# Kernel optimization log

Hardware: AMD Instinct MI355X
Metric: run time of the kernel (lower is better)

## Reference

```python
import jax, jax.numpy as jnp
import numpy as np
from jax import lax

# quantization bit widths (config)
IB, WB, RB, AB = 8, 4, 4, 8


def quantize(x, bw):
    """Signed fixed-point quantization to bw bits in [-1, 1) with STE."""
    scale = 2.0 ** (bw - 1)
    q = jnp.clip(jnp.round(x * scale), -scale, scale - 1) / scale
    return x + lax.stop_gradient(q - x)


def setup_inputs() -> dict:
    key = jax.random.key(0)
    k1, k2, k3, k4, k5 = jax.random.split(key, 5)
    B, T, I, H, O = 256, 1024, 64, 256, 16
    inputs = jax.random.normal(k1, (B, T, I), dtype=jnp.float32)
    # input kernel init: uniform(-1, 1)
    Wi = jax.random.uniform(k2, (H, I), dtype=jnp.float32, minval=-1.0, maxval=1.0)
    # recurrent kernel: orthogonal (geotorch parametrization); materialize via QR
    A = jax.random.normal(k3, (H, H), dtype=jnp.float32)
    Wr, _ = jnp.linalg.qr(A)
    Wr = Wr.astype(jnp.float32)
    Wo = jax.random.normal(k4, (O, H), dtype=jnp.float32) * 0.1
    b = jax.random.normal(k5, (H,), dtype=jnp.float32) * 0.01
    return {"inputs": inputs, "Wi": Wi, "Wr": Wr, "Wo": Wo, "b": b}


def reference(inputs, Wi, Wr, Wo, b):
    # quantize inputs (ib bits)
    x = quantize(inputs, IB)
    # quantized input projection, precomputed for all timesteps: [B,T,H]
    u = jnp.einsum("bti,hi->bth", x, quantize(Wi, WB))
    Wrq = quantize(Wr, RB)  # quantized orthogonal recurrent weight [H,H]
    B = inputs.shape[0]
    H = Wr.shape[0]
    h0 = jnp.zeros((B, H), dtype=inputs.dtype)

    def step(h, u_t):
        z = u_t + h @ Wrq.T                      # [B,H]
        m = jax.nn.relu(jnp.abs(z) + b)          # modrelu magnitude
        h_new = quantize(jnp.sign(z) * m, AB)    # quantized activation
        return h_new, None

    u_t = jnp.swapaxes(u, 0, 1)  # [T,B,H]
    h_last, _ = lax.scan(step, h0, u_t)
    # output head on last hidden state
    out = h_last @ quantize(Wo, WB).T  # [B,O]
    return out
```

## Files before the change

### kernel.cpp

```cpp
#include <hip/hip_runtime.h>


#define TSEQ 1024
#define IDIM 64
#define HDIM 256
#define ODIM 16

__device__ __forceinline__ int sdot4i8(int a, int b, int c) {
#if __has_builtin(__builtin_amdgcn_sdot4)
    return __builtin_amdgcn_sdot4(a, b, c, false);
#else
    int r = c;
    r += ((a << 24) >> 24) * ((b << 24) >> 24);
    r += ((a << 16) >> 24) * ((b << 16) >> 24);
    r += ((a << 8)  >> 24) * ((b << 8)  >> 24);
    r += (a >> 24) * (b >> 24);
    return r;
#endif
}

__device__ __forceinline__ int qpack4(float4 f, float s, float lo, float hi) {
    int a = (int)fminf(fmaxf(rintf(f.x * s), lo), hi);
    int b = (int)fminf(fmaxf(rintf(f.y * s), lo), hi);
    int c = (int)fminf(fmaxf(rintf(f.z * s), lo), hi);
    int d = (int)fminf(fmaxf(rintf(f.w * s), lo), hi);
    return (a & 255) | ((b & 255) << 8) | ((c & 255) << 16) | ((d & 255) << 24);
}

__device__ __forceinline__ int qsum(int v) {
    v += __builtin_amdgcn_update_dpp(0, v, 0xB1, 0xF, 0xF, true);
    v += __builtin_amdgcn_update_dpp(0, v, 0x4E, 0xF, 0xF, true);
    return v;
}

__global__ __launch_bounds__(256, 1)
void qornn_kernel(const float* __restrict__ x, const float* __restrict__ Wi,
                  const float* __restrict__ Wr, const float* __restrict__ Wo,
                  const float* __restrict__ bias, float* __restrict__ out) {
    __shared__ alignas(16) int xlds[TSEQ * 16 + 16];
    __shared__ alignas(16) int wstage[8192];
    __shared__ alignas(16) int hbuf[2][64];

    const int tid = threadIdx.x;
    const int brow = blockIdx.x;
    const int w    = tid >> 6;
    const int l    = tid & 63;
    const int q    = l & 3;
    const int m16  = l >> 2;
    const int obase = w * 64 + m16 * 4;

    {
        const float4* wi4 = (const float4*)Wi;
        #pragma unroll
        for (int it = 0; it < 16; ++it) {
            int flat = it * 256 + tid;
            wstage[flat] = qpack4(wi4[flat], 8.0f, -8.0f, 7.0f);
        }
    }
    __syncthreads();
    int4 wiq[4];
    {
        const int4* p = (const int4*)wstage;
        #pragma unroll
        for (int i = 0; i < 4; ++i) wiq[i] = p[(obase + i) * 4 + q];
    }
    __syncthreads();

    int4 wr[16];
    {
        const float4* wr4 = (const float4*)Wr;
        #pragma unroll
        for (int it = 0; it < 32; ++it) {
            int flat = it * 256 + tid;
            wstage[flat] = qpack4(wr4[flat], 8.0f, -8.0f, 7.0f);
        }
        __syncthreads();
        if (obase < 128) {
            const int4* p = (const int4*)wstage;
            #pragma unroll
            for (int i = 0; i < 4; ++i)
                #pragma unroll
                for (int r = 0; r < 4; ++r)
                    wr[i * 4 + r] = p[(obase + i) * 16 + q * 4 + r];
        }
        __syncthreads();
        #pragma unroll
        for (int it = 0; it < 32; ++it) {
            int flat = it * 256 + tid;
            wstage[flat] = qpack4(wr4[8192 + flat], 8.0f, -8.0f, 7.0f);
        }
        __syncthreads();
        if (obase >= 128) {
            const int4* p = (const int4*)wstage;
            #pragma unroll
            for (int i = 0; i < 4; ++i)
                #pragma unroll
                for (int r = 0; r < 4; ++r)
                    wr[i * 4 + r] = p[(obase - 128 + i) * 16 + q * 4 + r];
        }
        __syncthreads();
    }

    {
        const float4* wo4 = (const float4*)Wo;
        #pragma unroll
        for (int it = 0; it < 4; ++it) {
            int flat = it * 256 + tid;
            wstage[flat] = qpack4(wo4[flat], 8.0f, -8.0f, 7.0f);
        }
    }

    {
        const float4* rowf4 = (const float4*)(x + (size_t)brow * (TSEQ * IDIM));
        #pragma unroll 8
        for (int it = 0; it < 64; ++it) {
            int flat = it * 256 + tid;
            xlds[flat] = qpack4(rowf4[flat], 128.0f, -128.0f, 127.0f);
        }
    }
    if (tid < 64) hbuf[0][tid] = 0;
    __syncthreads();

    const float bv = bias[tid];
    const bool qb0 = (q & 1) != 0;
    const bool qb1 = (q & 2) != 0;

    int u[4];
    {
        const int4 xx = ((const int4*)xlds)[q];
        #pragma unroll
        for (int i = 0; i < 4; ++i) {
            int s = sdot4i8(xx.x, wiq[i].x, 0);
            s = sdot4i8(xx.y, wiq[i].y, s);
            s = sdot4i8(xx.z, wiq[i].z, s);
            u[i] = sdot4i8(xx.w, wiq[i].w, s);
        }
    }

    #pragma unroll 2
    for (int t = 0; t < TSEQ; ++t) {
        int4 hh[4];
        {
            const int4* hP = (const int4*)hbuf[t & 1];
            #pragma unroll
            for (int r = 0; r < 4; ++r) hh[r] = hP[q * 4 + r];
        }
        const int4 xn = ((const int4*)xlds)[(t + 1) * 4 + q];

        int za[4], zb[4];
        #pragma unroll
        for (int i = 0; i < 4; ++i) {
            int s0 = u[i];
            s0 = sdot4i8(hh[0].x, wr[i * 4 + 0].x, s0);
            s0 = sdot4i8(hh[0].y, wr[i * 4 + 0].y, s0);
            s0 = sdot4i8(hh[0].z, wr[i * 4 + 0].z, s0);
            s0 = sdot4i8(hh[0].w, wr[i * 4 + 0].w, s0);
            s0 = sdot4i8(hh[1].x, wr[i * 4 + 1].x, s0);
            s0 = sdot4i8(hh[1].y, wr[i * 4 + 1].y, s0);
            s0 = sdot4i8(hh[1].z, wr[i * 4 + 1].z, s0);
            s0 = sdot4i8(hh[1].w, wr[i * 4 + 1].w, s0);
            int s1 = 0;
            s1 = sdot4i8(hh[2].x, wr[i * 4 + 2].x, s1);
            s1 = sdot4i8(hh[2].y, wr[i * 4 + 2].y, s1);
            s1 = sdot4i8(hh[2].z, wr[i * 4 + 2].z, s1);
            s1 = sdot4i8(hh[2].w, wr[i * 4 + 2].w, s1);
            s1 = sdot4i8(hh[3].x, wr[i * 4 + 3].x, s1);
            s1 = sdot4i8(hh[3].y, wr[i * 4 + 3].y, s1);
            s1 = sdot4i8(hh[3].z, wr[i * 4 + 3].z, s1);
            s1 = sdot4i8(hh[3].w, wr[i * 4 + 3].w, s1);
            za[i] = s0; zb[i] = s1;
        }
        int un[4];
        #pragma unroll
        for (int i = 0; i < 4; ++i) {
            int s = sdot4i8(xn.x, wiq[i].x, 0);
            s = sdot4i8(xn.y, wiq[i].y, s);
            s = sdot4i8(xn.z, wiq[i].z, s);
            un[i] = sdot4i8(xn.w, wiq[i].w, s);
        }

        const int z0 = qsum(za[0] + zb[0]);
        const int z1 = qsum(za[1] + zb[1]);
        const int z2 = qsum(za[2] + zb[2]);
        const int z3 = qsum(za[3] + zb[3]);
        const int zlo = qb0 ? z1 : z0;
        const int zhi = qb0 ? z3 : z2;
        const int z   = qb1 ? zhi : zlo;

        const float zf = (float)z;
        const float t1 = fmaf(fabsf(zf), 0.0009765625f, bv);
        const float t2 = fmaxf(t1, 0.0f);
        const float r  = rintf(t2 * 128.0f);
        const int vpos = (int)fminf(r, 127.0f);
        const int vneg = -(int)fminf(r, 128.0f);
        int hv = (z < 0) ? vneg : vpos;
        hv = (z == 0) ? 0 : hv;

        ((signed char*)hbuf[(t + 1) & 1])[tid] = (signed char)hv;

        #pragma unroll
        for (int i = 0; i < 4; ++i) u[i] = un[i];
        __syncthreads();
    }

    if (tid < ODIM) {
        const int4* wo = (const int4*)wstage;
        const int4* hl = (const int4*)hbuf[0];
        int a0 = 0, a1 = 0, a2 = 0, a3 = 0;
        #pragma unroll
        for (int i = 0; i < 16; ++i) {
            int4 w4 = wo[tid * 16 + i];
            int4 h4 = hl[i];
            a0 = sdot4i8(h4.x, w4.x, a0);
            a1 = sdot4i8(h4.y, w4.y, a1);
            a2 = sdot4i8(h4.z, w4.z, a2);
            a3 = sdot4i8(h4.w, w4.w, a3);
        }
        out[brow * ODIM + tid] = (float)((a0 + a1) + (a2 + a3)) * 0.0009765625f;
    }
}

extern "C" void kernel_launch(void* const* d_in, const int* in_sizes, int n_in,
                              void* d_out, int out_size, void* d_ws, size_t ws_size,
                              hipStream_t stream) {
    const float* x  = (const float*)d_in[0];
    const float* Wi = (const float*)d_in[1];
    const float* Wr = (const float*)d_in[2];
    const float* Wo = (const float*)d_in[3];
    const float* b  = (const float*)d_in[4];
    float* out = (float*)d_out;

    const int B = in_sizes[0] / (TSEQ * IDIM);
    qornn_kernel<<<B, HDIM, 0, stream>>>(x, Wi, Wr, Wo, b, out);
}
```

Measured before the change: 423.1 us.

## Pack four batch rows per block and stream input chunks double-buffered

```diff
diff --git a/kernel.cpp b/kernel.cpp
--- a/kernel.cpp
+++ b/kernel.cpp
@@ -5,6 +5,9 @@
 #define IDIM 64
 #define HDIM 256
 #define ODIM 16
+#define RPW 4
+#define CHUNK 64
+#define NCHUNK (TSEQ / CHUNK)
 
 __device__ __forceinline__ int sdot4i8(int a, int b, int c) {
 #if __has_builtin(__builtin_amdgcn_sdot4)
@@ -33,27 +36,26 @@
     return v;
 }
 
-__global__ __launch_bounds__(256, 1)
+__global__ __launch_bounds__(1024, 1)
 void qornn_kernel(const float* __restrict__ x, const float* __restrict__ Wi,
                   const float* __restrict__ Wr, const float* __restrict__ Wo,
                   const float* __restrict__ bias, float* __restrict__ out) {
-    __shared__ alignas(16) int xlds[TSEQ * 16 + 16];
     __shared__ alignas(16) int wstage[8192];
-    __shared__ alignas(16) int hbuf[2][64];
-
-    const int tid = threadIdx.x;
-    const int brow = blockIdx.x;
-    const int w    = tid >> 6;
-    const int l    = tid & 63;
+    __shared__ alignas(16) int wo_lds[1024];
+    __shared__ alignas(16) int hbuf[RPW][2][64];
+
+    const int tid  = threadIdx.x;
+    const int g    = tid >> 8;
+    const int t256 = tid & 255;
+    const int l    = t256 & 63;
     const int q    = l & 3;
-    const int m16  = l >> 2;
-    const int obase = w * 64 + m16 * 4;
+    const int obase = (t256 >> 6) * 64 + (l >> 2) * 4;
 
     {
         const float4* wi4 = (const float4*)Wi;
         #pragma unroll
-        for (int it = 0; it < 16; ++it) {
-            int flat = it * 256 + tid;
+        for (int it = 0; it < 4; ++it) {
+            int flat = it * 1024 + tid;
             wstage[flat] = qpack4(wi4[flat], 8.0f, -8.0f, 7.0f);
         }
     }
@@ -70,64 +72,50 @@
     {
         const float4* wr4 = (const float4*)Wr;
         #pragma unroll
-        for (int it = 0; it < 32; ++it) {
-            int flat = it * 256 + tid;
-            wstage[flat] = qpack4(wr4[flat], 8.0f, -8.0f, 7.0f);
-        }
-        __syncthreads();
-        if (obase < 128) {
-            const int4* p = (const int4*)wstage;
+        for (int half = 0; half < 2; ++half) {
             #pragma unroll
-            for (int i = 0; i < 4; ++i)
+            for (int it = 0; it < 8; ++it) {
+                int flat = it * 1024 + tid;
+                wstage[flat] = qpack4(wr4[half * 8192 + flat], 8.0f, -8.0f, 7.0f);
+            }
+            __syncthreads();
+            if ((obase >> 7) == half) {
+                const int4* p = (const int4*)wstage;
+                const int ob = obase & 127;
                 #pragma unroll
-                for (int r = 0; r < 4; ++r)
-                    wr[i * 4 + r] = p[(obase + i) * 16 + q * 4 + r];
-        }
-        __syncthreads();
-        #pragma unroll
-        for (int it = 0; it < 32; ++it) {
-            int flat = it * 256 + tid;
-            wstage[flat] = qpack4(wr4[8192 + flat], 8.0f, -8.0f, 7.0f);
-        }
-        __syncthreads();
-        if (obase >= 128) {
-            const int4* p = (const int4*)wstage;
-            #pragma unroll
-            for (int i = 0; i < 4; ++i)
-                #pragma unroll
-                for (int r = 0; r < 4; ++r)
-                    wr[i * 4 + r] = p[(obase - 128 + i) * 16 + q * 4 + r];
-        }
-        __syncthreads();
+                for (int i = 0; i < 4; ++i)
+                    #pragma unroll
+                    for (int r = 0; r < 4; ++r)
+                        wr[i * 4 + r] = p[(ob + i) * 16 + q * 4 + r];
+            }
+            __syncthreads();
+        }
     }
 
     {
         const float4* wo4 = (const float4*)Wo;
+        wo_lds[tid] = qpack4(wo4[tid], 8.0f, -8.0f, 7.0f);
+    }
+
+    const int row = blockIdx.x * RPW + g;
+    const float4* rowf4 = (const float4*)(x + (size_t)row * (TSEQ * IDIM));
+    int* xg = wstage + g * 2048;
+    {
         #pragma unroll
         for (int it = 0; it < 4; ++it) {
-            int flat = it * 256 + tid;
-            wstage[flat] = qpack4(wo4[flat], 8.0f, -8.0f, 7.0f);
-        }
-    }
-
-    {
-        const float4* rowf4 = (const float4*)(x + (size_t)brow * (TSEQ * IDIM));
-        #pragma unroll 8
-        for (int it = 0; it < 64; ++it) {
-            int flat = it * 256 + tid;
-            xlds[flat] = qpack4(rowf4[flat], 128.0f, -128.0f, 127.0f);
-        }
-    }
-    if (tid < 64) hbuf[0][tid] = 0;
-    __syncthreads();
-
-    const float bv = bias[tid];
+            int idx = it * 256 + t256;
+            xg[idx] = qpack4(rowf4[idx], 128.0f, -128.0f, 127.0f);
+        }
+    }
+    if (t256 < 64) hbuf[g][0][t256] = 0;
+    const float bv = bias[t256];
     const bool qb0 = (q & 1) != 0;
     const bool qb1 = (q & 2) != 0;
+    __syncthreads();
 
     int u[4];
     {
-        const int4 xx = ((const int4*)xlds)[q];
+        const int4 xx = *(const int4*)(xg + q * 4);
         #pragma unroll
         for (int i = 0; i < 4; ++i) {
             int s = sdot4i8(xx.x, wiq[i].x, 0);
@@ -137,15 +125,25 @@
         }
     }
 
-    #pragma unroll 2
     for (int t = 0; t < TSEQ; ++t) {
+        if ((t & (CHUNK - 1)) == (g << 3) && t < TSEQ - CHUNK) {
+            const int nc = (t >> 6) + 1;
+            int* dst = xg + (nc & 1) * 1024;
+            #pragma unroll
+            for (int it = 0; it < 4; ++it) {
+                int idx = it * 256 + t256;
+                dst[idx] = qpack4(rowf4[nc * 1024 + idx], 128.0f, -128.0f, 127.0f);
+            }
+        }
+
         int4 hh[4];
         {
-            const int4* hP = (const int4*)hbuf[t & 1];
+            const int4* hP = (const int4*)hbuf[g][t & 1];
             #pragma unroll
             for (int r = 0; r < 4; ++r) hh[r] = hP[q * 4 + r];
         }
-        const int4 xn = ((const int4*)xlds)[(t + 1) * 4 + q];
+        const int tt = (t + 1) & (TSEQ - 1);
+        const int4 xn = *(const int4*)(xg + ((tt >> 6) & 1) * 1024 + (tt & 63) * 16 + q * 4);
 
         int za[4], zb[4];
         #pragma unroll
@@ -196,27 +194,27 @@
         int hv = (z < 0) ? vneg : vpos;
         hv = (z == 0) ? 0 : hv;
 
-        ((signed char*)hbuf[(t + 1) & 1])[tid] = (signed char)hv;
+        ((signed char*)hbuf[g][(t + 1) & 1])[t256] = (signed char)hv;
 
         #pragma unroll
         for (int i = 0; i < 4; ++i) u[i] = un[i];
         __syncthreads();
     }
 
-    if (tid < ODIM) {
-        const int4* wo = (const int4*)wstage;
-        const int4* hl = (const int4*)hbuf[0];
+    if (t256 < ODIM) {
+        const int4* wo = (const int4*)wo_lds;
+        const int4* hl = (const int4*)hbuf[g][0];
         int a0 = 0, a1 = 0, a2 = 0, a3 = 0;
         #pragma unroll
         for (int i = 0; i < 16; ++i) {
-            int4 w4 = wo[tid * 16 + i];
+            int4 w4 = wo[t256 * 16 + i];
             int4 h4 = hl[i];
             a0 = sdot4i8(h4.x, w4.x, a0);
             a1 = sdot4i8(h4.y, w4.y, a1);
             a2 = sdot4i8(h4.z, w4.z, a2);
             a3 = sdot4i8(h4.w, w4.w, a3);
         }
-        out[brow * ODIM + tid] = (float)((a0 + a1) + (a2 + a3)) * 0.0009765625f;
+        out[row * ODIM + t256] = (float)((a0 + a1) + (a2 + a3)) * 0.0009765625f;
     }
 }
 
@@ -231,5 +229,5 @@
     float* out = (float*)d_out;
 
     const int B = in_sizes[0] / (TSEQ * IDIM);
-    qornn_kernel<<<B, HDIM, 0, stream>>>(x, Wi, Wr, Wo, b, out);
-}
+    qornn_kernel<<<B / RPW, RPW * 256, 0, stream>>>(x, Wi, Wr, Wo, b, out);
+}
```

Result: slower. 1.091 ms (+158.0%).

## Double threads per block, halving output rows per quad in recurrence

Applied to the files above, without the earlier changes.

```diff
diff --git a/kernel.cpp b/kernel.cpp
--- a/kernel.cpp
+++ b/kernel.cpp
@@ -33,103 +33,88 @@
     return v;
 }
 
-__global__ __launch_bounds__(256, 1)
+__global__ __launch_bounds__(512, 2)
 void qornn_kernel(const float* __restrict__ x, const float* __restrict__ Wi,
                   const float* __restrict__ Wr, const float* __restrict__ Wo,
                   const float* __restrict__ bias, float* __restrict__ out) {
     __shared__ alignas(16) int xlds[TSEQ * 16 + 16];
     __shared__ alignas(16) int wstage[8192];
+    __shared__ alignas(16) int wo_lds[1024];
     __shared__ alignas(16) int hbuf[2][64];
 
     const int tid = threadIdx.x;
     const int brow = blockIdx.x;
-    const int w    = tid >> 6;
-    const int l    = tid & 63;
-    const int q    = l & 3;
-    const int m16  = l >> 2;
-    const int obase = w * 64 + m16 * 4;
+    const int l   = tid & 63;
+    const int wv  = tid >> 6;
+    const int q   = l & 3;
+    const int Q   = wv * 16 + (l >> 2);
+    const int obase = Q * 2;
+    const int osel  = q & 1;
 
     {
         const float4* wi4 = (const float4*)Wi;
         #pragma unroll
-        for (int it = 0; it < 16; ++it) {
-            int flat = it * 256 + tid;
+        for (int it = 0; it < 8; ++it) {
+            int flat = it * 512 + tid;
             wstage[flat] = qpack4(wi4[flat], 8.0f, -8.0f, 7.0f);
         }
     }
     __syncthreads();
-    int4 wiq[4];
+    int4 wiq[2];
     {
         const int4* p = (const int4*)wstage;
         #pragma unroll
-        for (int i = 0; i < 4; ++i) wiq[i] = p[(obase + i) * 4 + q];
+        for (int i = 0; i < 2; ++i) wiq[i] = p[(obase + i) * 4 + q];
     }
     __syncthreads();
 
-    int4 wr[16];
+    int4 wr[8];
     {
         const float4* wr4 = (const float4*)Wr;
         #pragma unroll
-        for (int it = 0; it < 32; ++it) {
-            int flat = it * 256 + tid;
-            wstage[flat] = qpack4(wr4[flat], 8.0f, -8.0f, 7.0f);
-        }
-        __syncthreads();
-        if (obase < 128) {
-            const int4* p = (const int4*)wstage;
+        for (int half = 0; half < 2; ++half) {
             #pragma unroll
-            for (int i = 0; i < 4; ++i)
+            for (int it = 0; it < 16; ++it) {
+                int flat = it * 512 + tid;
+                wstage[flat] = qpack4(wr4[half * 8192 + flat], 8.0f, -8.0f, 7.0f);
+            }
+            __syncthreads();
+            if ((obase >> 7) == half) {
+                const int4* p = (const int4*)wstage;
+                const int ob = obase & 127;
                 #pragma unroll
-                for (int r = 0; r < 4; ++r)
-                    wr[i * 4 + r] = p[(obase + i) * 16 + q * 4 + r];
-        }
-        __syncthreads();
-        #pragma unroll
-        for (int it = 0; it < 32; ++it) {
-            int flat = it * 256 + tid;
-            wstage[flat] = qpack4(wr4[8192 + flat], 8.0f, -8.0f, 7.0f);
-        }
-        __syncthreads();
-        if (obase >= 128) {
-            const int4* p = (const int4*)wstage;
-            #pragma unroll
-            for (int i = 0; i < 4; ++i)
-                #pragma unroll
-                for (int r = 0; r < 4; ++r)
-                    wr[i * 4 + r] = p[(obase - 128 + i) * 16 + q * 4 + r];
-        }
-        __syncthreads();
+                for (int i = 0; i < 2; ++i)
+                    #pragma unroll
+                    for (int r = 0; r < 4; ++r)
+                        wr[i * 4 + r] = p[(ob + i) * 16 + q * 4 + r];
+            }
+            __syncthreads();
+        }
     }
 
     {
         const float4* wo4 = (const float4*)Wo;
-        #pragma unroll
-        for (int it = 0; it < 4; ++it) {
-            int flat = it * 256 + tid;
-            wstage[flat] = qpack4(wo4[flat], 8.0f, -8.0f, 7.0f);
-        }
+        wo_lds[tid]       = qpack4(wo4[tid],       8.0f, -8.0f, 7.0f);
+        wo_lds[tid + 512] = qpack4(wo4[tid + 512], 8.0f, -8.0f, 7.0f);
     }
 
     {
         const float4* rowf4 = (const float4*)(x + (size_t)brow * (TSEQ * IDIM));
         #pragma unroll 8
-        for (int it = 0; it < 64; ++it) {
-            int flat = it * 256 + tid;
+        for (int it = 0; it < 32; ++it) {
+            int flat = it * 512 + tid;
             xlds[flat] = qpack4(rowf4[flat], 128.0f, -128.0f, 127.0f);
         }
     }
     if (tid < 64) hbuf[0][tid] = 0;
+    const float bv = bias[obase + osel];
     __syncthreads();
 
-    const float bv = bias[tid];
-    const bool qb0 = (q & 1) != 0;
-    const bool qb1 = (q & 2) != 0;
-
-    int u[4];
+    int u[2];
     {
         const int4 xx = ((const int4*)xlds)[q];
         #pragma unroll
-        for (int i = 0; i < 4; ++i) {
+        for (int i = 0; i < 2; ++i) {
             int s = sdot4i8(xx.x, wiq[i].x, 0);
             s = sdot4i8(xx.y, wiq[i].y, s);
             s = sdot4i8(xx.z, wiq[i].z, s);
@@ -137,7 +122,6 @@
         }
     }
 
-    #pragma unroll 2
     for (int t = 0; t < TSEQ; ++t) {
         int4 hh[4];
         {
@@ -147,9 +131,9 @@
         }
         const int4 xn = ((const int4*)xlds)[(t + 1) * 4 + q];
 
-        int za[4], zb[4];
-        #pragma unroll
-        for (int i = 0; i < 4; ++i) {
+        int za[2], zb[2];
+        #pragma unroll
+        for (int i = 0; i < 2; ++i) {
             int s0 = u[i];
             s0 = sdot4i8(hh[0].x, wr[i * 4 + 0].x, s0);
             s0 = sdot4i8(hh[0].y, wr[i * 4 + 0].y, s0);
@@ -170,9 +154,9 @@
             s1 = sdot4i8(hh[3].w, wr[i * 4 + 3].w, s1);
             za[i] = s0; zb[i] = s1;
         }
-        int un[4];
-        #pragma unroll
-        for (int i = 0; i < 4; ++i) {
+        int un[2];
+        #pragma unroll
+        for (int i = 0; i < 2; ++i) {
             int s = sdot4i8(xn.x, wiq[i].x, 0);
             s = sdot4i8(xn.y, wiq[i].y, s);
             s = sdot4i8(xn.z, wiq[i].z, s);
@@ -181,11 +165,7 @@
 
         const int z0 = qsum(za[0] + zb[0]);
         const int z1 = qsum(za[1] + zb[1]);
-        const int z2 = qsum(za[2] + zb[2]);
-        const int z3 = qsum(za[3] + zb[3]);
-        const int zlo = qb0 ? z1 : z0;
-        const int zhi = qb0 ? z3 : z2;
-        const int z   = qb1 ? zhi : zlo;
+        const int z  = osel ? z1 : z0;
 
         const float zf = (float)z;
         const float t1 = fmaf(fabsf(zf), 0.0009765625f, bv);
@@ -196,15 +176,14 @@
         int hv = (z < 0) ? vneg : vpos;
         hv = (z == 0) ? 0 : hv;
 
-        ((signed char*)hbuf[(t + 1) & 1])[tid] = (signed char)hv;
-
-        #pragma unroll
-        for (int i = 0; i < 4; ++i) u[i] = un[i];
+        if (q < 2) ((signed char*)hbuf[(t + 1) & 1])[obase + osel] = (signed char)hv;
+
+        u[0] = un[0]; u[1] = un[1];
         __syncthreads();
     }
 
     if (tid < ODIM) {
-        const int4* wo = (const int4*)wstage;
+        const int4* wo = (const int4*)wo_lds;
         const int4* hl = (const int4*)hbuf[0];
         int a0 = 0, a1 = 0, a2 = 0, a3 = 0;
         #pragma unroll
@@ -231,5 +210,5 @@
     float* out = (float*)d_out;
 
     const int B = in_sizes[0] / (TSEQ * IDIM);
-    qornn_kernel<<<B, HDIM, 0, stream>>>(x, Wi, Wr, Wo, b, out);
-}
+    qornn_kernel<<<B, 512, 0, stream>>>(x, Wi, Wr, Wo, b, out);
+}
```

New measurement: 513.8 us. 21.4% more time.
